# Kernel optimization log

Hardware: AMD Instinct MI355X
Metric: run time of the kernel (lower is better)

Reference implementation:

```python
import jax, jax.numpy as jnp
import numpy as np

ACT_SCALE = 0.02            # activation_scale from init
ACT_QMIN = -(2 ** 15)       # activation_bits=16
ACT_QMAX = 2 ** 15 - 1


def setup_inputs() -> dict:
    key = jax.random.key(0)
    k_x, k_w, k_s, k_b = jax.random.split(key, 4)
    B, S, IN, OUT = 4, 2048, 4096, 11008
    x = jax.random.normal(k_x, (B, S, IN), dtype=jnp.float32)
    # int8-range weights stored as int32 buffer (torch.randint default int)
    weight = jax.random.randint(k_w, (OUT, IN), -128, 128, dtype=jnp.int32)
    scale = jax.random.normal(k_s, (OUT,), dtype=jnp.float32)
    bias = jax.random.normal(k_b, (1, OUT), dtype=jnp.float32)
    return {"x": x, "weight": weight, "scale": scale, "bias": bias}


def reference(x, weight, scale, bias):
    # quantize activations: round(x / activation_scale), clamp to int16 range
    x_int = jnp.clip(jnp.round(x / ACT_SCALE), ACT_QMIN, ACT_QMAX)
    # F.linear(x_int, weight.to(x.dtype)) : [B,S,IN] @ [OUT,IN]^T -> [B,S,OUT]
    out_int = jnp.einsum('bsi,oi->bso', x_int, weight.astype(x.dtype))
    # per-output-channel dequant + bias (bias shape [1,OUT] broadcasts)
    return out_int * (ACT_SCALE * scale) + bias
```

## Files before the change

### kernel.cpp

```cpp
#include <hip/hip_runtime.h>
#include <stdint.h>

typedef _Float16 half_t;
typedef _Float16 half8 __attribute__((ext_vector_type(8)));
typedef _Float16 half4v __attribute__((ext_vector_type(4)));
typedef float floatx4 __attribute__((ext_vector_type(4)));

#define M_TOT 8192
#define N_TOT 11008
#define K_TOT 4096

__global__ __launch_bounds__(256) void quantize_kernel(
    const float* __restrict__ x, half_t* __restrict__ xq) {
  int i = blockIdx.x * blockDim.x + threadIdx.x;
  float4 v = ((const float4*)x)[i];
  float q0 = fminf(fmaxf(rintf(v.x / 0.02f), -32768.f), 32767.f);
  float q1 = fminf(fmaxf(rintf(v.y / 0.02f), -32768.f), 32767.f);
  float q2 = fminf(fmaxf(rintf(v.z / 0.02f), -32768.f), 32767.f);
  float q3 = fminf(fmaxf(rintf(v.w / 0.02f), -32768.f), 32767.f);
  half4v h;
  h.x = (half_t)q0; h.y = (half_t)q1; h.z = (half_t)q2; h.w = (half_t)q3;
  ((half4v*)xq)[i] = h;
}

__global__ __launch_bounds__(256) void wconv_kernel(
    const int* __restrict__ w, half_t* __restrict__ wf) {
  int i = blockIdx.x * blockDim.x + threadIdx.x;
  int4 v = ((const int4*)w)[i];
  half4v h;
  h.x = (half_t)(float)v.x; h.y = (half_t)(float)v.y;
  h.z = (half_t)(float)v.z; h.w = (half_t)(float)v.w;
  ((half4v*)wf)[i] = h;
}

__device__ __forceinline__ void async16(const half_t* g, half_t* l) {
  __builtin_amdgcn_global_load_lds(
      (const __attribute__((address_space(1))) void*)g,
      (__attribute__((address_space(3))) void*)l, 16, 0, 0);
}

#define VMCNT(N) asm volatile("s_waitcnt vmcnt(" #N ")" ::: "memory")
#define BARX()                               \
  do {                                       \
    __builtin_amdgcn_s_barrier();            \
    __builtin_amdgcn_sched_barrier(0);       \
  } while (0)

__global__ __launch_bounds__(512) void gemm_kernel(
    const half_t* __restrict__ A,
    const half_t* __restrict__ W,
    const float* __restrict__ scale,
    const float* __restrict__ bias,
    float* __restrict__ C) {
  __shared__ __align__(16) half_t lds[65536];

  const int tid = threadIdx.x;
  const int lane = tid & 63;
  const int wave = tid >> 6;
  const int wm = wave >> 2;
  const int wn = wave & 3;

  int id = blockIdx.x;
  id = (id & 7) * 172 + (id >> 3);
  const int bm = ((id / 172) * 4 + ((id % 172) & 3)) * 256;
  const int bn = ((id % 172) >> 2) * 256;

  const int c0 = tid, c1 = tid + 512;
  const int r0 = c0 >> 2, r1 = c1 >> 2;
  const int kc0 = (c0 & 3) ^ ((r0 >> 1) & 3);
  const int kc1 = (c1 & 3) ^ ((r1 >> 1) & 3);
  const half_t* agA0 = A + (size_t)(bm + r0) * K_TOT + kc0 * 8;
  const half_t* agA1 = A + (size_t)(bm + r1) * K_TOT + kc1 * 8;
  const half_t* agB0 = W + (size_t)(bn + r0) * K_TOT + kc0 * 8;
  const half_t* agB1 = W + (size_t)(bn + r1) * K_TOT + kc1 * 8;

#define STAGE_A(S, KOFF)                                  \
  do {                                                    \
    async16(agA0 + (KOFF), lds + (S)*8192 + c0 * 8);      \
    async16(agA1 + (KOFF), lds + (S)*8192 + c1 * 8);      \
  } while (0)
#define STAGE_B(S, KOFF)                                          \
  do {                                                            \
    async16(agB0 + (KOFF), lds + 32768 + (S)*8192 + c0 * 8);      \
    async16(agB1 + (KOFF), lds + 32768 + (S)*8192 + c1 * 8);      \
  } while (0)
#define NOSTAGE() (void)0
#define NOWAIT() (void)0

  const int fr = lane & 15;
  const int kcs = (lane >> 4) ^ ((fr >> 1) & 3);
  const int aoff = (wm * 128 + fr) * 32 + kcs * 8;
  const int boff = 32768 + (wn * 64 + fr) * 32 + kcs * 8;

  floatx4 acc[8][4] = {};

#define PHASE(QM, CS, STAGE_STMT, WAIT_STMT)                              \
  do {                                                                    \
    half8 af[4], wf[4];                                                   \
    const half_t* ap = lds + (CS)*8192 + aoff + (QM)*2048;                \
    const half_t* bp = lds + (CS)*8192 + boff;                            \
    _Pragma("unroll") for (int i = 0; i < 4; ++i)                         \
        af[i] = *(const half8*)(ap + i * 512);                            \
    _Pragma("unroll") for (int j = 0; j < 4; ++j)                         \
        wf[j] = *(const half8*)(bp + j * 512);                            \
    STAGE_STMT;                                                           \
    WAIT_STMT;                                                            \
    BARX();                                                               \
    __builtin_amdgcn_s_setprio(1);                                        \
    _Pragma("unroll") for (int i = 0; i < 4; ++i)                         \
        _Pragma("unroll") for (int j = 0; j < 4; ++j)                     \
            acc[(QM)*4 + i][j] = __builtin_amdgcn_mfma_f32_16x16x32_f16(  \
                af[i], wf[j], acc[(QM)*4 + i][j], 0, 0, 0);               \
    __builtin_amdgcn_s_setprio(0);                                        \
    BARX();                                                               \
  } while (0)

  STAGE_A(0, 0);  STAGE_B(0, 0);
  STAGE_A(1, 32); STAGE_B(1, 32);
  STAGE_A(2, 64); STAGE_B(2, 64);
  VMCNT(6);
  BARX();

  for (int it = 0; it < 31; ++it) {
    const int kb = it * 128;
    PHASE(0, 0, STAGE_A(3, kb + 96),  NOWAIT());
    PHASE(1, 0, STAGE_B(3, kb + 96),  VMCNT(6));
    PHASE(0, 1, STAGE_A(0, kb + 128), NOWAIT());
    PHASE(1, 1, STAGE_B(0, kb + 128), VMCNT(6));
    PHASE(0, 2, STAGE_A(1, kb + 160), NOWAIT());
    PHASE(1, 2, STAGE_B(1, kb + 160), VMCNT(6));
    PHASE(0, 3, STAGE_A(2, kb + 192), NOWAIT());
    PHASE(1, 3, STAGE_B(2, kb + 192), VMCNT(6));
  }

  PHASE(0, 0, STAGE_A(3, 4064), NOWAIT());
  PHASE(1, 0, STAGE_B(3, 4064), VMCNT(6));
  PHASE(0, 1, NOSTAGE(), NOWAIT());
  PHASE(1, 1, NOSTAGE(), VMCNT(4));
  PHASE(0, 2, NOSTAGE(), NOWAIT());
  PHASE(1, 2, NOSTAGE(), VMCNT(0));
  PHASE(0, 3, NOSTAGE(), NOWAIT());
  PHASE(1, 3, NOSTAGE(), NOWAIT());

  const int row0 = bm + wm * 128 + (lane >> 4) * 4;
  const int col0 = bn + wn * 64 + (lane & 15);
#pragma unroll
  for (int j = 0; j < 4; ++j) {
    const int col = col0 + j * 16;
    const float alpha = 0.02f * scale[col];
    const float beta = bias[col];
#pragma unroll
    for (int i8 = 0; i8 < 8; ++i8) {
      float* cp = C + (size_t)(row0 + i8 * 16) * N_TOT + col;
#pragma unroll
      for (int r = 0; r < 4; ++r)
        cp[(size_t)r * N_TOT] = acc[i8][j][r] * alpha + beta;
    }
  }
}

extern "C" void kernel_launch(void* const* d_in, const int* in_sizes, int n_in,
                              void* d_out, int out_size, void* d_ws,
                              size_t ws_size, hipStream_t stream) {
  const float* x = (const float*)d_in[0];
  const int* w = (const int*)d_in[1];
  const float* scale = (const float*)d_in[2];
  const float* bias = (const float*)d_in[3];
  float* out = (float*)d_out;

  half_t* xq = (half_t*)d_ws;
  half_t* wq = (half_t*)((char*)d_ws + (size_t)M_TOT * K_TOT * sizeof(half_t));

  quantize_kernel<<<32768, 256, 0, stream>>>(x, xq);
  wconv_kernel<<<44032, 256, 0, stream>>>(w, wq);

  gemm_kernel<<<1376, 512, 0, stream>>>(xq, wq, scale, bias, out);
}
```

Measured before the change: 1.198 ms.

## Double-buffer GEMM fragments in registers and cut barriers per k-stage

```diff
diff --git a/kernel.cpp b/kernel.cpp
--- a/kernel.cpp
+++ b/kernel.cpp
@@ -89,58 +89,61 @@
 
   const int fr = lane & 15;
   const int kcs = (lane >> 4) ^ ((fr >> 1) & 3);
-  const int aoff = (wm * 128 + fr) * 32 + kcs * 8;
-  const int boff = 32768 + (wn * 64 + fr) * 32 + kcs * 8;
+  const half_t* abase = lds + (wm * 128 + fr) * 32 + kcs * 8;
+  const half_t* bbase = lds + 32768 + (wn * 64 + fr) * 32 + kcs * 8;
 
+  half8 wf[4], af0[4], af1[4];
   floatx4 acc[8][4] = {};
 
-#define PHASE(QM, CS, STAGE_STMT, WAIT_STMT)                              \
+#define BODY(S, SN, STGA, STGB, ROLL, WAIT)                               \
   do {                                                                    \
-    half8 af[4], wf[4];                                                   \
-    const half_t* ap = lds + (CS)*8192 + aoff + (QM)*2048;                \
-    const half_t* bp = lds + (CS)*8192 + boff;                            \
+    BARX();                                                               \
     _Pragma("unroll") for (int i = 0; i < 4; ++i)                         \
-        af[i] = *(const half8*)(ap + i * 512);                            \
-    _Pragma("unroll") for (int j = 0; j < 4; ++j)                         \
-        wf[j] = *(const half8*)(bp + j * 512);                            \
-    STAGE_STMT;                                                           \
-    WAIT_STMT;                                                            \
-    BARX();                                                               \
+        af1[i] = *(const half8*)(abase + (S)*8192 + 2048 + i * 512);      \
+    STGA;                                                                 \
     __builtin_amdgcn_s_setprio(1);                                        \
-    _Pragma("unroll") for (int i = 0; i < 4; ++i)                         \
-        _Pragma("unroll") for (int j = 0; j < 4; ++j)                     \
-            acc[(QM)*4 + i][j] = __builtin_amdgcn_mfma_f32_16x16x32_f16(  \
-                af[i], wf[j], acc[(QM)*4 + i][j], 0, 0, 0);               \
+    _Pragma("unroll") for (int i = 0; i < 4; ++i) {                       \
+      _Pragma("unroll") for (int j = 0; j < 4; ++j)                       \
+          acc[i][j] = __builtin_amdgcn_mfma_f32_16x16x32_f16(             \
+              af0[i], wf[j], acc[i][j], 0, 0, 0);                         \
+      if (ROLL)                                                           \
+        af0[i] = *(const half8*)(abase + (SN)*8192 + i * 512);            \
+    }                                                                     \
     __builtin_amdgcn_s_setprio(0);                                        \
-    BARX();                                                               \
+    STGB;                                                                 \
+    __builtin_amdgcn_s_setprio(1);                                        \
+    _Pragma("unroll") for (int j = 0; j < 4; ++j) {                       \
+      _Pragma("unroll") for (int i = 0; i < 4; ++i)                       \
+          acc[4 + i][j] = __builtin_amdgcn_mfma_f32_16x16x32_f16(         \
+              af1[i], wf[j], acc[4 + i][j], 0, 0, 0);                     \
+      if (ROLL)                                                           \
+        wf[j] = *(const half8*)(bbase + (SN)*8192 + j * 512);             \
+    }                                                                     \
+    __builtin_amdgcn_s_setprio(0);                                        \
+    WAIT;                                                                 \
   } while (0)
 
   STAGE_A(0, 0);  STAGE_B(0, 0);
   STAGE_A(1, 32); STAGE_B(1, 32);
   STAGE_A(2, 64); STAGE_B(2, 64);
-  VMCNT(6);
+  VMCNT(4);
   BARX();
+#pragma unroll
+  for (int j = 0; j < 4; ++j) wf[j] = *(const half8*)(bbase + j * 512);
+#pragma unroll
+  for (int i = 0; i < 4; ++i) af0[i] = *(const half8*)(abase + i * 512);
 
   for (int it = 0; it < 31; ++it) {
     const int kb = it * 128;
-    PHASE(0, 0, STAGE_A(3, kb + 96),  NOWAIT());
-    PHASE(1, 0, STAGE_B(3, kb + 96),  VMCNT(6));
-    PHASE(0, 1, STAGE_A(0, kb + 128), NOWAIT());
-    PHASE(1, 1, STAGE_B(0, kb + 128), VMCNT(6));
-    PHASE(0, 2, STAGE_A(1, kb + 160), NOWAIT());
-    PHASE(1, 2, STAGE_B(1, kb + 160), VMCNT(6));
-    PHASE(0, 3, STAGE_A(2, kb + 192), NOWAIT());
-    PHASE(1, 3, STAGE_B(2, kb + 192), VMCNT(6));
+    BODY(0, 1, STAGE_A(3, kb + 96),  STAGE_B(3, kb + 96),  true, VMCNT(4));
+    BODY(1, 2, STAGE_A(0, kb + 128), STAGE_B(0, kb + 128), true, VMCNT(4));
+    BODY(2, 3, STAGE_A(1, kb + 160), STAGE_B(1, kb + 160), true, VMCNT(4));
+    BODY(3, 0, STAGE_A(2, kb + 192), STAGE_B(2, kb + 192), true, VMCNT(4));
   }
-
-  PHASE(0, 0, STAGE_A(3, 4064), NOWAIT());
-  PHASE(1, 0, STAGE_B(3, 4064), VMCNT(6));
-  PHASE(0, 1, NOSTAGE(), NOWAIT());
-  PHASE(1, 1, NOSTAGE(), VMCNT(4));
-  PHASE(0, 2, NOSTAGE(), NOWAIT());
-  PHASE(1, 2, NOSTAGE(), VMCNT(0));
-  PHASE(0, 3, NOSTAGE(), NOWAIT());
-  PHASE(1, 3, NOSTAGE(), NOWAIT());
+  BODY(0, 1, STAGE_A(3, 4064), STAGE_B(3, 4064), true,  VMCNT(4));
+  BODY(1, 2, NOSTAGE(),        NOSTAGE(),        true,  VMCNT(0));
+  BODY(2, 3, NOSTAGE(),        NOSTAGE(),        true,  NOWAIT());
+  BODY(3, 0, NOSTAGE(),        NOSTAGE(),        false, NOWAIT());
 
   const int row0 = bm + wm * 128 + (lane >> 4) * 4;
   const int col0 = bn + wn * 64 + (lane & 15);
```

Result: faster. 1.143 ms (-4.6%).
